# Kernel optimization log

Hardware: AMD Instinct MI355X
Metric: run time of the kernel (lower is better)

The kernel has to match this reference:

```python
import jax, jax.numpy as jnp
import numpy as np

B, T, D, U = 32, 4096, 512, 256

def setup_inputs() -> dict:
    key = jax.random.key(0)
    ks = jax.random.split(key, 5)
    s = 1.0 / np.sqrt(D)
    return {
        "values": jax.random.normal(ks[0], (B, T, D), dtype=jnp.float32),
        "query": jax.random.normal(ks[1], (B, D), dtype=jnp.float32),
        "W1": jax.random.normal(ks[2], (D, U), dtype=jnp.float32) * s,
        "b1": jnp.zeros((U,), dtype=jnp.float32),
        "W2": jax.random.normal(ks[3], (D, U), dtype=jnp.float32) * s,
        "b2": jnp.zeros((U,), dtype=jnp.float32),
        "V": jax.random.normal(ks[4], (U, 1), dtype=jnp.float32) * (1.0 / np.sqrt(U)),
        "bV": jnp.zeros((1,), dtype=jnp.float32),
    }

def reference(values, query, W1, b1, W2, b2, V, bV):
    # values: [B,T,D], query: [B,D]
    h_vals = jnp.einsum('btd,du->btu', values, W1) + b1          # [B,T,U]
    h_query = (query @ W2 + b2)[:, None, :]                       # [B,1,U]
    score = jnp.einsum('btu,uo->bto', jnp.tanh(h_vals + h_query), V) + bV  # [B,T,1]
    attention_weights = jax.nn.softmax(score, axis=1)             # [B,T,1]
    context_vector = jnp.sum(attention_weights * values, axis=1)  # [B,D]
    return context_vector, attention_weights
```

## Files before the change

### kernel.cpp

```cpp
#include <hip/hip_runtime.h>
#include <math.h>
#include <stdint.h>

#define BB 32
#define TT 4096
#define DD 512
#define UU 256

#define KC 32
#define NKC (DD/KC)
#define LDA 40
#define NTILE (TT/64)

typedef __attribute__((ext_vector_type(8))) short short8;
typedef __attribute__((ext_vector_type(8))) unsigned short ushort8;
typedef __attribute__((ext_vector_type(4))) float floatx4;

__device__ __forceinline__ unsigned short bf16_rne(float x) {
  union { float f; uint32_t u; } v; v.f = x;
  uint32_t r = v.u + 0x7FFFu + ((v.u >> 16) & 1u);
  return (unsigned short)(r >> 16);
}
__device__ __forceinline__ float tanh_fast(float x) {
  float e = __expf(2.0f * x);
  return 1.0f - 2.0f * __builtin_amdgcn_rcpf(e + 1.0f);
}

__global__ __launch_bounds__(256) void prep_w1_kernel(
    const float* __restrict__ W1, unsigned short* __restrict__ w1t) {
  const int kc = blockIdx.x;
  const int u = threadIdx.x;
  __attribute__((aligned(16))) unsigned short row[KC];
#pragma unroll
  for (int kk = 0; kk < KC; ++kk)
    row[kk] = bf16_rne(W1[(kc * KC + kk) * UU + u]);
  unsigned short* dst = w1t + ((size_t)kc * UU + u) * KC;
#pragma unroll
  for (int i = 0; i < 4; ++i) ((uint4*)dst)[i] = *(const uint4*)&row[i * 8];
}

__global__ __launch_bounds__(256) void hquery_kernel(
    const float* __restrict__ query, const float* __restrict__ W2,
    const float* __restrict__ b2, const float* __restrict__ b1,
    float* __restrict__ hq) {
  const int b = blockIdx.x;
  const int u = threadIdx.x;
  __shared__ float qs[DD];
  for (int d = threadIdx.x; d < DD; d += 256) qs[d] = query[b * DD + d];
  __syncthreads();
  float acc = b2[u] + b1[u];
  for (int d = 0; d < DD; ++d) acc += qs[d] * W2[d * UU + u];
  hq[b * UU + u] = acc;
}

__global__ __launch_bounds__(256) void score_kernel(
    const float* __restrict__ values, const unsigned short* __restrict__ w1t,
    const float* __restrict__ hq, const float* __restrict__ V,
    const float* __restrict__ bV, float* __restrict__ scores,
    float* __restrict__ pml, float* __restrict__ pctx) {
  const int b = blockIdx.y;
  const int blk = blockIdx.x;
  const int t0 = blk * 64;
  const int tid = threadIdx.x;
  const int wave = tid >> 6;
  const int lane = tid & 63;
  const int c = lane & 15;
  const int q = lane >> 4;

  __shared__ unsigned short As[2][64 * LDA];
  __shared__ float redW[4][64];
  __shared__ float warr[64];

  floatx4 acc[4][4];
#pragma unroll
  for (int ti = 0; ti < 4; ++ti)
#pragma unroll
    for (int ui = 0; ui < 4; ++ui) acc[ti][ui] = (floatx4){0.f, 0.f, 0.f, 0.f};

  const int ar = tid >> 2;
  const int aseg = tid & 3;
  const float* asrc =
      values + ((size_t)b * TT + t0 + ar) * DD + aseg * 8;

  const unsigned short* bbase = w1t + ((size_t)(wave * 64 + c)) * KC + q * 8;

  float4 aq[2][2];
  aq[0][0] = *(const float4*)(asrc);
  aq[0][1] = *(const float4*)(asrc + 4);
  aq[1][0] = *(const float4*)(asrc + KC);
  aq[1][1] = *(const float4*)(asrc + KC + 4);

  for (int kc = 0; kc < NKC; ++kc) {
    const int buf = kc & 1;
    {
      const float4 f0 = aq[buf][0], f1 = aq[buf][1];
      ushort8 t8;
      t8[0] = bf16_rne(f0.x); t8[1] = bf16_rne(f0.y);
      t8[2] = bf16_rne(f0.z); t8[3] = bf16_rne(f0.w);
      t8[4] = bf16_rne(f1.x); t8[5] = bf16_rne(f1.y);
      t8[6] = bf16_rne(f1.z); t8[7] = bf16_rne(f1.w);
      *(ushort8*)&As[buf][ar * LDA + aseg * 8] = t8;
    }
    __syncthreads();

    short8 bfr[4];
#pragma unroll
    for (int ui = 0; ui < 4; ++ui)
      bfr[ui] = *(const short8*)(bbase + ((size_t)kc * UU + ui * 16) * KC);
    short8 afr[4];
#pragma unroll
    for (int ti = 0; ti < 4; ++ti)
      afr[ti] = *(const short8*)&As[buf][(ti * 16 + c) * LDA + q * 8];

    if (kc + 2 < NKC) {
      aq[buf][0] = *(const float4*)(asrc + (kc + 2) * KC);
      aq[buf][1] = *(const float4*)(asrc + (kc + 2) * KC + 4);
    }

#pragma unroll
    for (int ti = 0; ti < 4; ++ti)
#pragma unroll
      for (int ui = 0; ui < 4; ++ui)
        acc[ti][ui] = __builtin_amdgcn_mfma_f32_16x16x32_bf16(
            afr[ti], bfr[ui], acc[ti][ui], 0, 0, 0);
  }

  float hqv[4], vv[4];
#pragma unroll
  for (int ui = 0; ui < 4; ++ui) {
    const int u = wave * 64 + ui * 16 + c;
    hqv[ui] = hq[b * UU + u];
    vv[ui] = V[u];
  }
#pragma unroll
  for (int ti = 0; ti < 4; ++ti)
#pragma unroll
    for (int r = 0; r < 4; ++r) {
      float e = 0.0f;
#pragma unroll
      for (int ui = 0; ui < 4; ++ui)
        e += tanh_fast(acc[ti][ui][r] + hqv[ui]) * vv[ui];
      e += __shfl_xor(e, 1, 64);
      e += __shfl_xor(e, 2, 64);
      e += __shfl_xor(e, 4, 64);
      e += __shfl_xor(e, 8, 64);
      if (c == 0) redW[wave][ti * 16 + q * 4 + r] = e;
    }
  __syncthreads();
  if (tid < 64) {
    const float s =
        bV[0] + redW[0][tid] + redW[1][tid] + redW[2][tid] + redW[3][tid];
    scores[b * TT + t0 + tid] = s;
    redW[0][tid] = s;
  }
  __syncthreads();
  float mb = -1e30f;
#pragma unroll 8
  for (int t = 0; t < 64; ++t) mb = fmaxf(mb, redW[0][t]);
  if (tid < 64) warr[tid] = __expf(redW[0][tid] - mb);
  __syncthreads();
  float lb = 0.0f;
#pragma unroll 8
  for (int t = 0; t < 64; ++t) lb += warr[t];

  const float2* vp = (const float2*)(values + ((size_t)b * TT + t0) * DD);
  float2 c2 = {0.f, 0.f};
#pragma unroll 4
  for (int t = 0; t < 64; ++t) {
    const float w = warr[t];
    const float2 v = vp[(size_t)t * (DD / 2) + tid];
    c2.x += w * v.x;
    c2.y += w * v.y;
  }
  *(float2*)&pctx[((size_t)b * NTILE + blk) * DD + 2 * tid] = c2;
  if (tid == 0) {
    pml[(b * NTILE + blk) * 2 + 0] = mb;
    pml[(b * NTILE + blk) * 2 + 1] = lb;
  }
}

__global__ __launch_bounds__(256) void combine_kernel(
    const float* __restrict__ pml, const float* __restrict__ pctx,
    float* __restrict__ out, float* __restrict__ stats) {
  const int b = blockIdx.x;
  const int tid = threadIdx.x;
  __shared__ float mls[2 * NTILE];
  __shared__ float cs[NTILE];
  if (tid < 2 * NTILE) mls[tid] = pml[b * 2 * NTILE + tid];
  __syncthreads();
  float m = -1e30f;
#pragma unroll 8
  for (int i = 0; i < NTILE; ++i) m = fmaxf(m, mls[2 * i]);
  if (tid < NTILE) cs[tid] = __expf(mls[2 * tid] - m);
  __syncthreads();
  float l = 0.0f;
#pragma unroll 8
  for (int i = 0; i < NTILE; ++i) l += cs[i] * mls[2 * i + 1];

  const float2* pp = (const float2*)(pctx + (size_t)b * NTILE * DD);
  float2 acc = {0.f, 0.f};
#pragma unroll 4
  for (int i = 0; i < NTILE; ++i) {
    const float cw = cs[i];
    const float2 p = pp[(size_t)i * (DD / 2) + tid];
    acc.x += cw * p.x;
    acc.y += cw * p.y;
  }
  const float linv = 1.0f / l;
  out[b * DD + 2 * tid + 0] = acc.x * linv;
  out[b * DD + 2 * tid + 1] = acc.y * linv;
  if (tid == 0) {
    stats[2 * b + 0] = m;
    stats[2 * b + 1] = l;
  }
}

__global__ __launch_bounds__(256) void weights_kernel(
    const float* __restrict__ scores, const float* __restrict__ stats,
    float* __restrict__ out) {
  const int b = blockIdx.y;
  const int t = blockIdx.x * 256 + threadIdx.x;
  const float m = stats[2 * b];
  const float linv = 1.0f / stats[2 * b + 1];
  out[BB * DD + b * TT + t] = __expf(scores[b * TT + t] - m) * linv;
}

extern "C" void kernel_launch(void* const* d_in, const int* in_sizes, int n_in,
                              void* d_out, int out_size, void* d_ws, size_t ws_size,
                              hipStream_t stream) {
  const float* values = (const float*)d_in[0];
  const float* query  = (const float*)d_in[1];
  const float* W1     = (const float*)d_in[2];
  const float* b1     = (const float*)d_in[3];
  const float* W2     = (const float*)d_in[4];
  const float* b2     = (const float*)d_in[5];
  const float* V      = (const float*)d_in[6];
  const float* bV     = (const float*)d_in[7];
  float* out = (float*)d_out;

  float* ws = (float*)d_ws;
  float* hq     = ws;
  float* scores = ws + BB * UU;
  float* stats  = scores + BB * TT;
  float* pml    = stats + 2 * BB;
  float* pctx   = pml + BB * NTILE * 2;
  unsigned short* w1t = (unsigned short*)(pctx + (size_t)BB * NTILE * DD);

  prep_w1_kernel<<<NKC, 256, 0, stream>>>(W1, w1t);
  hquery_kernel<<<BB, 256, 0, stream>>>(query, W2, b2, b1, hq);
  score_kernel<<<dim3(NTILE, BB), 256, 0, stream>>>(
      values, w1t, hq, V, bV, scores, pml, pctx);
  combine_kernel<<<BB, 256, 0, stream>>>(pml, pctx, out, stats);
  weights_kernel<<<dim3(TT / 256, BB), 256, 0, stream>>>(scores, stats, out);
}
```

Measured before the change: 455.7 us.

## Fuse setup and weight kernels, double-buffer W1 fragments in score loop

Merges the W1 conversion and query projection into one setup launch, and folds the softmax-weight normalization into the combine kernel, removing two launches and the stats buffer. In the score kernel the W1 fragments for the next k-chunk are prefetched into a second register buffer, the k-loop is fully unrolled, and the sync is replaced by an LDS-only wait plus barrier. This is meant to hide global-load latency of B fragments behind MFMAs. The cost is higher register pressure, and the combine kernel now does more serial work per block with only 32 blocks.

```diff
diff --git a/kernel.cpp b/kernel.cpp
--- a/kernel.cpp
+++ b/kernel.cpp
@@ -26,31 +26,43 @@
   return 1.0f - 2.0f * __builtin_amdgcn_rcpf(e + 1.0f);
 }
 
-__global__ __launch_bounds__(256) void prep_w1_kernel(
-    const float* __restrict__ W1, unsigned short* __restrict__ w1t) {
-  const int kc = blockIdx.x;
-  const int u = threadIdx.x;
-  __attribute__((aligned(16))) unsigned short row[KC];
-#pragma unroll
-  for (int kk = 0; kk < KC; ++kk)
-    row[kk] = bf16_rne(W1[(kc * KC + kk) * UU + u]);
-  unsigned short* dst = w1t + ((size_t)kc * UU + u) * KC;
-#pragma unroll
-  for (int i = 0; i < 4; ++i) ((uint4*)dst)[i] = *(const uint4*)&row[i * 8];
-}
-
-__global__ __launch_bounds__(256) void hquery_kernel(
+#define BAR_LDS()                                     \
+  do {                                                \
+    asm volatile("s_waitcnt lgkmcnt(0)" ::: "memory");\
+    __builtin_amdgcn_s_barrier();                     \
+  } while (0)
+
+__global__ __launch_bounds__(256) void setup_kernel(
+    const float* __restrict__ W1, unsigned short* __restrict__ w1t,
     const float* __restrict__ query, const float* __restrict__ W2,
     const float* __restrict__ b2, const float* __restrict__ b1,
     float* __restrict__ hq) {
-  const int b = blockIdx.x;
-  const int u = threadIdx.x;
   __shared__ float qs[DD];
-  for (int d = threadIdx.x; d < DD; d += 256) qs[d] = query[b * DD + d];
-  __syncthreads();
-  float acc = b2[u] + b1[u];
-  for (int d = 0; d < DD; ++d) acc += qs[d] * W2[d * UU + u];
-  hq[b * UU + u] = acc;
+  if (blockIdx.x < NKC) {
+    const int kc = blockIdx.x;
+    const int u = threadIdx.x;
+    __attribute__((aligned(16))) unsigned short row[KC];
+#pragma unroll
+    for (int kk = 0; kk < KC; ++kk)
+      row[kk] = bf16_rne(W1[(kc * KC + kk) * UU + u]);
+    unsigned short* dst = w1t + ((size_t)kc * UU + u) * KC;
+#pragma unroll
+    for (int i = 0; i < 4; ++i) ((uint4*)dst)[i] = *(const uint4*)&row[i * 8];
+  } else {
+    const int b = blockIdx.x - NKC;
+    const int u = threadIdx.x;
+    for (int d = threadIdx.x; d < DD; d += 256) qs[d] = query[b * DD + d];
+    __syncthreads();
+    float a0 = 0.f, a1 = 0.f, a2 = 0.f, a3 = 0.f;
+#pragma unroll 4
+    for (int d = 0; d < DD; d += 4) {
+      a0 += qs[d + 0] * W2[(d + 0) * UU + u];
+      a1 += qs[d + 1] * W2[(d + 1) * UU + u];
+      a2 += qs[d + 2] * W2[(d + 2) * UU + u];
+      a3 += qs[d + 3] * W2[(d + 3) * UU + u];
+    }
+    hq[b * UU + u] = (a0 + a1) + (a2 + a3) + b2[u] + b1[u];
+  }
 }
 
 __global__ __launch_bounds__(256) void score_kernel(
@@ -85,11 +97,17 @@
   const unsigned short* bbase = w1t + ((size_t)(wave * 64 + c)) * KC + q * 8;
 
   float4 aq[2][2];
+  short8 bfr[2][4];
+
   aq[0][0] = *(const float4*)(asrc);
   aq[0][1] = *(const float4*)(asrc + 4);
   aq[1][0] = *(const float4*)(asrc + KC);
   aq[1][1] = *(const float4*)(asrc + KC + 4);
-
+#pragma unroll
+  for (int ui = 0; ui < 4; ++ui)
+    bfr[0][ui] = *(const short8*)(bbase + (size_t)(ui * 16) * KC);
+
+#pragma unroll
   for (int kc = 0; kc < NKC; ++kc) {
     const int buf = kc & 1;
     {
@@ -101,28 +119,27 @@
       t8[6] = bf16_rne(f1.z); t8[7] = bf16_rne(f1.w);
       *(ushort8*)&As[buf][ar * LDA + aseg * 8] = t8;
     }
-    __syncthreads();
-
-    short8 bfr[4];
-#pragma unroll
-    for (int ui = 0; ui < 4; ++ui)
-      bfr[ui] = *(const short8*)(bbase + ((size_t)kc * UU + ui * 16) * KC);
-    short8 afr[4];
-#pragma unroll
-    for (int ti = 0; ti < 4; ++ti)
-      afr[ti] = *(const short8*)&As[buf][(ti * 16 + c) * LDA + q * 8];
-
     if (kc + 2 < NKC) {
       aq[buf][0] = *(const float4*)(asrc + (kc + 2) * KC);
       aq[buf][1] = *(const float4*)(asrc + (kc + 2) * KC + 4);
     }
-
+    BAR_LDS();
+    short8 afr[4];
+#pragma unroll
+    for (int ti = 0; ti < 4; ++ti)
+      afr[ti] = *(const short8*)&As[buf][(ti * 16 + c) * LDA + q * 8];
+    if (kc + 1 < NKC) {
+#pragma unroll
+      for (int ui = 0; ui < 4; ++ui)
+        bfr[buf ^ 1][ui] =
+            *(const short8*)(bbase + ((size_t)(kc + 1) * UU + ui * 16) * KC);
+    }
 #pragma unroll
     for (int ti = 0; ti < 4; ++ti)
 #pragma unroll
       for (int ui = 0; ui < 4; ++ui)
         acc[ti][ui] = __builtin_amdgcn_mfma_f32_16x16x32_bf16(
-            afr[ti], bfr[ui], acc[ti][ui], 0, 0, 0);
+            afr[ti], bfr[buf][ui], acc[ti][ui], 0, 0, 0);
   }
 
   float hqv[4], vv[4];
@@ -181,7 +198,7 @@
 
 __global__ __launch_bounds__(256) void combine_kernel(
     const float* __restrict__ pml, const float* __restrict__ pctx,
-    float* __restrict__ out, float* __restrict__ stats) {
+    const float* __restrict__ scores, float* __restrict__ out) {
   const int b = blockIdx.x;
   const int tid = threadIdx.x;
   __shared__ float mls[2 * NTILE];
@@ -196,6 +213,7 @@
   float l = 0.0f;
 #pragma unroll 8
   for (int i = 0; i < NTILE; ++i) l += cs[i] * mls[2 * i + 1];
+  const float linv = 1.0f / l;
 
   const float2* pp = (const float2*)(pctx + (size_t)b * NTILE * DD);
   float2 acc = {0.f, 0.f};
@@ -206,23 +224,16 @@
     acc.x += cw * p.x;
     acc.y += cw * p.y;
   }
-  const float linv = 1.0f / l;
   out[b * DD + 2 * tid + 0] = acc.x * linv;
   out[b * DD + 2 * tid + 1] = acc.y * linv;
-  if (tid == 0) {
-    stats[2 * b + 0] = m;
-    stats[2 * b + 1] = l;
-  }
-}
-
-__global__ __launch_bounds__(256) void weights_kernel(
-    const float* __restrict__ scores, const float* __restrict__ stats,
-    float* __restrict__ out) {
-  const int b = blockIdx.y;
-  const int t = blockIdx.x * 256 + threadIdx.x;
-  const float m = stats[2 * b];
-  const float linv = 1.0f / stats[2 * b + 1];
-  out[BB * DD + b * TT + t] = __expf(scores[b * TT + t] - m) * linv;
+
+  float* wout = out + BB * DD + (size_t)b * TT;
+  const float* srow = scores + (size_t)b * TT;
+#pragma unroll
+  for (int i = 0; i < TT / 256; ++i) {
+    const int t = i * 256 + tid;
+    wout[t] = __expf(srow[t] - m) * linv;
+  }
 }
 
 extern "C" void kernel_launch(void* const* d_in, const int* in_sizes, int n_in,
@@ -241,15 +252,12 @@
   float* ws = (float*)d_ws;
   float* hq     = ws;
   float* scores = ws + BB * UU;
-  float* stats  = scores + BB * TT;
-  float* pml    = stats + 2 * BB;
+  float* pml    = scores + BB * TT;
   float* pctx   = pml + BB * NTILE * 2;
   unsigned short* w1t = (unsigned short*)(pctx + (size_t)BB * NTILE * DD);
 
-  prep_w1_kernel<<<NKC, 256, 0, stream>>>(W1, w1t);
-  hquery_kernel<<<BB, 256, 0, stream>>>(query, W2, b2, b1, hq);
+  setup_kernel<<<NKC + BB, 256, 0, stream>>>(W1, w1t, query, W2, b2, b1, hq);
   score_kernel<<<dim3(NTILE, BB), 256, 0, stream>>>(
       values, w1t, hq, V, bV, scores, pml, pctx);
-  combine_kernel<<<BB, 256, 0, stream>>>(pml, pctx, out, stats);
-  weights_kernel<<<dim3(TT / 256, BB), 256, 0, stream>>>(scores, stats, out);
-}
+  combine_kernel<<<BB, 256, 0, stream>>>(pml, pctx, scores, out);
+}
```

Measured after the change: 441.2 us. 1.03x faster.
